# Kernel tuning notes

Measured on AMD Instinct MI355X. Metric: run time of the kernel, lower is better.

The kernel has to match this reference:

```python
import jax, jax.numpy as jnp
import numpy as np

N = 50000
E_RAND = 800000
E = E_RAND + N  # random edges + self loops
IN_DIM = 128
H = 4
D = 32  # num_hidden
HD = H * D  # 128
N_CLS = 2
NEG_SLOPE = 0.2
BN_EPS = 1e-5


def setup_inputs() -> dict:
    key = jax.random.key(0)
    ks = jax.random.split(key, 32)
    x = jax.random.randint(ks[0], (N,), 0, 200)
    src_r = jax.random.randint(ks[1], (E_RAND,), 0, N)
    dst_r = jax.random.randint(ks[2], (E_RAND,), 0, N)
    loops = jnp.arange(N)
    src = jnp.concatenate([src_r, loops])
    dst = jnp.concatenate([dst_r, loops])
    snorm_n = jax.random.uniform(ks[3], (N, 1), jnp.float32, 0.1, 1.0)
    snorm_e = jax.random.uniform(ks[4], (E, 1), jnp.float32, 0.1, 1.0)

    def nrm(k, shape, fan_in):
        return jax.random.normal(k, shape, jnp.float32) * (1.0 / np.sqrt(fan_in))

    inp = {
        'x': x, 'src': src, 'dst': dst, 'snorm_n': snorm_n, 'snorm_e': snorm_e,
        'embed': nrm(ks[5], (200, IN_DIM), 1.0),
        'W0': nrm(ks[6], (IN_DIM, HD), IN_DIM),
        'al0': nrm(ks[7], (H, D), D), 'ar0': nrm(ks[8], (H, D), D),
        'gamma0': jnp.ones((HD,), jnp.float32), 'beta0': jnp.zeros((HD,), jnp.float32),
        'W1': nrm(ks[9], (HD, HD), HD),
        'al1': nrm(ks[10], (H, D), D), 'ar1': nrm(ks[11], (H, D), D),
        'gamma1': jnp.ones((HD,), jnp.float32), 'beta1': jnp.zeros((HD,), jnp.float32),
        'W2': nrm(ks[12], (HD, HD), HD),
        'al2': nrm(ks[13], (H, D), D), 'ar2': nrm(ks[14], (H, D), D),
        'gamma2': jnp.ones((HD,), jnp.float32), 'beta2': jnp.zeros((HD,), jnp.float32),
        'cls1_w': nrm(ks[15], (HD, HD // 2), HD), 'cls1_b': jnp.zeros((HD // 2,), jnp.float32),
        'cls2_w': nrm(ks[16], (HD // 2, N_CLS), HD // 2), 'cls2_b': jnp.zeros((N_CLS,), jnp.float32),
    }
    return inp


def _gat_conv(h, W, al, ar, src, dst, residual, apply_act):
    # h: [N, F_in]; DGL-style GATConv with edge softmax over destination.
    feat = (h @ W).reshape(N, H, D)                         # [N,H,D]
    el = jnp.sum(feat * al, axis=-1)                        # [N,H]
    er = jnp.sum(feat * ar, axis=-1)                        # [N,H]
    e = jax.nn.leaky_relu(el[src] + er[dst], NEG_SLOPE)     # [E,H]
    m = jax.ops.segment_max(e, dst, num_segments=N)         # per-dst max
    ee = jnp.exp(e - m[dst])
    s = jax.ops.segment_sum(ee, dst, num_segments=N)
    a = ee / s[dst]                                         # edge softmax [E,H]
    msg = feat[src] * a[:, :, None]                         # [E,H,D]
    rst = jax.ops.segment_sum(msg, dst, num_segments=N)     # [N,H,D]
    if residual:
        rst = rst + h.reshape(N, H, D)  # identity residual (dims match)
    if apply_act:
        rst = jax.nn.elu(rst)           # activation inside GATConv (layers > 0)
    return rst.reshape(N, HD)


def _bn(h, gamma, beta):
    mu = jnp.mean(h, axis=0)
    var = jnp.mean((h - mu) ** 2, axis=0)  # biased var, matches torch BN training
    return gamma * (h - mu) * jax.lax.rsqrt(var + BN_EPS) + beta


def reference(x, src, dst, snorm_n, snorm_e, embed,
              W0, al0, ar0, gamma0, beta0,
              W1, al1, ar1, gamma1, beta1,
              W2, al2, ar2, gamma2, beta2,
              cls1_w, cls1_b, cls2_w, cls2_b):
    h = embed[x]  # [N, IN_DIM]
    layers = [
        (W0, al0, ar0, gamma0, beta0, False, False),
        (W1, al1, ar1, gamma1, beta1, True, True),
        (W2, al2, ar2, gamma2, beta2, True, True),
    ]
    for W, al, ar, g, b, res, act in layers:
        h = _gat_conv(h, W, al, ar, src, dst, res, act)
        h = h * snorm_n
        h = _bn(h, g, b)
        h = jax.nn.elu(h)
    h = jax.nn.relu(h @ cls1_w + cls1_b)
    logits = h @ cls2_w + cls2_b  # [N, N_CLS]
    return logits
```

## Files before the change

### kernel.cpp

```cpp
#include <hip/hip_runtime.h>
#include <hip/hip_bf16.h>
#include <hip/hip_fp16.h>
#include <math.h>

constexpr int N_NODES = 50000;
constexpr int N_EDGES = 850000;
constexpr int HDIM = 128;
constexpr int AGG_BLOCKS = N_NODES / 8;
constexpr int BN_BUCKETS = 16;

typedef _Float16 f16x8 __attribute__((ext_vector_type(8)));
typedef float f32x4 __attribute__((ext_vector_type(4)));

#define FMAMIX_LO(acc, pk, w) \
    asm("v_fma_mix_f32 %0, %1, %2, %0 op_sel:[0,0,0] op_sel_hi:[1,0,0]" \
        : "+v"(acc) : "v"(pk), "v"(w))
#define FMAMIX_HI(acc, pk, w) \
    asm("v_fma_mix_f32 %0, %1, %2, %0 op_sel:[1,0,0] op_sel_hi:[1,0,0]" \
        : "+v"(acc) : "v"(pk), "v"(w))

__device__ __forceinline__ float elu1(float t) {
    return (t > 0.f) ? t : (__expf(t) - 1.f);
}

constexpr int NB2 = 128;
constexpr int RANGE2 = (N_NODES + NB2 - 1) / NB2;
constexpr int CAP = 8192;
constexpr int CHUNK = 8192;
constexpr int GA = (N_EDGES + CHUNK - 1) / CHUNK;

__global__ void k_partA(const int* __restrict__ src, const int* __restrict__ dst,
                        int* __restrict__ g_cursor, unsigned* __restrict__ bucket) {
    __shared__ int hist[NB2];
    int tid = threadIdx.x;
    int e0 = blockIdx.x * CHUNK;
    int e1 = min(e0 + CHUNK, N_EDGES);
    if (tid < NB2) hist[tid] = 0;
    __syncthreads();
    for (int i = e0 + tid; i < e1; i += 1024) {
        int d = dst[i];
        atomicAdd(&hist[d / RANGE2], 1);
    }
    __syncthreads();
    int base = 0;
    if (tid < NB2) base = atomicAdd(&g_cursor[tid], hist[tid]);
    __syncthreads();
    if (tid < NB2) hist[tid] = base;
    __syncthreads();
    for (int i = e0 + tid; i < e1; i += 1024) {
        int d = dst[i];
        int s = src[i];
        int b = d / RANGE2;
        int p = atomicAdd(&hist[b], 1);
        bucket[b * CAP + p] = (unsigned)s | ((unsigned)(d - b * RANGE2) << 16);
    }
}

__global__ void k_partB(const unsigned* __restrict__ bucket, const int* __restrict__ cnts,
                        int* __restrict__ rowstart, int* __restrict__ esrc) {
    __shared__ int cnt_s[NB2];
    __shared__ int hist[RANGE2];
    __shared__ int lcur[RANGE2];
    __shared__ int wsum[7];
    int b = blockIdx.x, tid = threadIdx.x;
    int lo = b * RANGE2;
    int myCount = cnts[b];
    if (tid < NB2) cnt_s[tid] = cnts[tid];
    __syncthreads();
    for (int off = 1; off < NB2; off <<= 1) {
        int t = (tid < NB2 && tid >= off) ? cnt_s[tid - off] : 0;
        __syncthreads();
        if (tid < NB2) cnt_s[tid] += t;
        __syncthreads();
    }
    int base = cnt_s[b] - myCount;
    for (int j = tid; j < RANGE2; j += 1024) hist[j] = 0;
    __syncthreads();
    const unsigned* my = bucket + (size_t)b * CAP;
    for (int i = tid; i < myCount; i += 1024) atomicAdd(&hist[my[i] >> 16], 1);
    __syncthreads();
    int v = 0;
    if (tid < 448) v = (tid < RANGE2) ? hist[tid] : 0;
    int inc = v;
    int lane = tid & 63;
#pragma unroll
    for (int off = 1; off < 64; off <<= 1) {
        int t = __shfl_up(inc, off, 64);
        if (lane >= off) inc += t;
    }
    if (tid < 448 && lane == 63) wsum[tid >> 6] = inc;
    __syncthreads();
    if (tid < RANGE2) {
        int woff = 0;
        for (int w = 0; w < (tid >> 6); w++) woff += wsum[w];
        int excl = woff + inc - v;
        lcur[tid] = excl;
        int node = lo + tid;
        if (node < N_NODES) rowstart[node] = base + excl;
    }
    if (b == 0 && tid == 0) rowstart[N_NODES] = N_EDGES;
    __syncthreads();
    for (int i = tid; i < myCount; i += 1024) {
        unsigned p = my[i];
        int pos = atomicAdd(&lcur[p >> 16], 1);
        esrc[base + pos] = (int)(p & 0xFFFFu);
    }
}

__global__ void k_wpack(const float* __restrict__ W0, const float* __restrict__ W1,
                        const float* __restrict__ W2, __half* __restrict__ wpk,
                        float* __restrict__ bn_part, int* __restrict__ g_cursor) {
    int gid = blockIdx.x * 256 + threadIdx.x;
    {
        int z0 = gid * 8;
        if (z0 < 3 * BN_BUCKETS * 256) {
            float4 z = make_float4(0.f, 0.f, 0.f, 0.f);
            *reinterpret_cast<float4*>(&bn_part[z0]) = z;
            *reinterpret_cast<float4*>(&bn_part[z0 + 4]) = z;
        }
        if (gid < NB2) g_cursor[gid] = 0;
    }
    if (gid >= 3 * 2048) return;
    int L = gid >> 11;
    int rem = gid & 2047;
    int ct = rem >> 8;
    int kc = (rem >> 6) & 3;
    int l = rem & 63;
    const float* W = (L == 0) ? W0 : ((L == 1) ? W1 : W2);
    int c = ct * 16 + (l & 15);
    int k0 = kc * 32 + (l >> 4) * 8;
    __half tmp[8];
#pragma unroll
    for (int j = 0; j < 8; j++) tmp[j] = __float2half(W[(k0 + j) * HDIM + c]);
    *reinterpret_cast<float4*>(&wpk[((size_t)L << 14) + ((size_t)(ct * 4 + kc) * 64 + l) * 8]) =
        *reinterpret_cast<float4*>(tmp);
}

__global__ void k_gemm6(const __half* __restrict__ h, const int* __restrict__ xidx,
                        const float* __restrict__ embed, const f16x8* __restrict__ wB,
                        __half* __restrict__ feat_h, const float* __restrict__ bn_prev,
                        const float* __restrict__ gamma, const float* __restrict__ beta,
                        const float* __restrict__ al, const float* __restrict__ ar,
                        float* __restrict__ el, float* __restrict__ er, int mode) {
    __shared__ __half sf[4][16][136];
    __shared__ __align__(16) float s_sc[128];
    __shared__ __align__(16) float s_sh[128];
    int tid = threadIdx.x;
    if (mode != 0) {
        float* red = reinterpret_cast<float*>(sf);
        int c = tid & 127, which = tid >> 7;
        float t = 0.f;
#pragma unroll
        for (int b = 0; b < BN_BUCKETS; b++) t += bn_prev[b * 256 + which * 128 + c];
        red[tid] = t;
        __syncthreads();
        if (tid < 128) {
            float mu = red[tid] * (1.f / N_NODES);
            float var = red[128 + tid] * (1.f / N_NODES) - mu * mu;
            float sc = gamma[tid] * rsqrtf(var + 1e-5f);
            s_sc[tid] = sc;
            s_sh[tid] = beta[tid] - mu * sc;
        }
        __syncthreads();
    }
    int w = tid >> 6, lane = tid & 63;
    int r = lane & 15, kg = lane >> 4;
    int wbase = blockIdx.x * 64 + w * 16;
    int n = wbase + r;
    bool ok = n < N_NODES;

    f16x8 aF[4];
#pragma unroll
    for (int kc = 0; kc < 4; kc++)
#pragma unroll
        for (int j = 0; j < 8; j++) aF[kc][j] = (_Float16)0.f;
    if (ok) {
        if (mode == 0) {
            int xi = xidx[n];
            const float* ep = embed + (size_t)xi * HDIM;
#pragma unroll
            for (int kc = 0; kc < 4; kc++) {
                int c0 = kc * 32 + kg * 8;
                float4 e0 = *reinterpret_cast<const float4*>(ep + c0);
                float4 e1 = *reinterpret_cast<const float4*>(ep + c0 + 4);
                aF[kc][0] = (_Float16)e0.x; aF[kc][1] = (_Float16)e0.y;
                aF[kc][2] = (_Float16)e0.z; aF[kc][3] = (_Float16)e0.w;
                aF[kc][4] = (_Float16)e1.x; aF[kc][5] = (_Float16)e1.y;
                aF[kc][6] = (_Float16)e1.z; aF[kc][7] = (_Float16)e1.w;
            }
        } else {
            const __half* hp = h + (size_t)n * HDIM;
#pragma unroll
            for (int kc = 0; kc < 4; kc++) {
                int c0 = kc * 32 + kg * 8;
                float4 raw = *reinterpret_cast<const float4*>(hp + c0);
                const __half2* u = reinterpret_cast<const __half2*>(&raw);
                float4 sc0 = *reinterpret_cast<const float4*>(&s_sc[c0]);
                float4 sc1 = *reinterpret_cast<const float4*>(&s_sc[c0 + 4]);
                float4 sh0 = *reinterpret_cast<const float4*>(&s_sh[c0]);
                float4 sh1 = *reinterpret_cast<const float4*>(&s_sh[c0 + 4]);
                float scv[8] = {sc0.x, sc0.y, sc0.z, sc0.w, sc1.x, sc1.y, sc1.z, sc1.w};
                float shv[8] = {sh0.x, sh0.y, sh0.z, sh0.w, sh1.x, sh1.y, sh1.z, sh1.w};
                float vv[8];
#pragma unroll
                for (int t = 0; t < 4; t++) {
                    vv[2 * t] = __half2float(__low2half(u[t]));
                    vv[2 * t + 1] = __half2float(__high2half(u[t]));
                }
#pragma unroll
                for (int j = 0; j < 8; j++) {
                    float t = vv[j] * scv[j] + shv[j];
                    aF[kc][j] = (_Float16)elu1(t);
                }
            }
        }
    }
    if (mode != 0) __syncthreads();

    f32x4 acc[8] = {};
#pragma unroll
    for (int kc = 0; kc < 4; kc++) {
#pragma unroll
        for (int ct = 0; ct < 8; ct++) {
            f16x8 bF = wB[(ct * 4 + kc) * 64 + lane];
            acc[ct] = __builtin_amdgcn_mfma_f32_16x16x32_f16(aF[kc], bF, acc[ct], 0, 0, 0);
        }
    }

#pragma unroll
    for (int ct = 0; ct < 8; ct++)
#pragma unroll
        for (int reg = 0; reg < 4; reg++)
            sf[w][kg * 4 + reg][ct * 16 + r] = __float2half(acc[ct][reg]);
    __syncthreads();
#pragma unroll
    for (int q = 0; q < 4; q++) {
        int row = q * 4 + kg;
        int n2 = wbase + row;
        if (n2 < N_NODES) {
            float4 v = *reinterpret_cast<const float4*>(&sf[w][row][r * 8]);
            *reinterpret_cast<float4*>(&feat_h[(size_t)n2 * HDIM + r * 8]) = v;
        }
    }

    float alq[8], arq[8];
#pragma unroll
    for (int ct = 0; ct < 8; ct++) {
        alq[ct] = al[ct * 16 + r];
        arq[ct] = ar[ct * 16 + r];
    }
#pragma unroll
    for (int hd = 0; hd < 4; hd++) {
        float pl[4], pr[4];
#pragma unroll
        for (int reg = 0; reg < 4; reg++) {
            pl[reg] = acc[2 * hd][reg] * alq[2 * hd] + acc[2 * hd + 1][reg] * alq[2 * hd + 1];
            pr[reg] = acc[2 * hd][reg] * arq[2 * hd] + acc[2 * hd + 1][reg] * arq[2 * hd + 1];
        }
#pragma unroll
        for (int off = 1; off < 16; off <<= 1)
#pragma unroll
            for (int reg = 0; reg < 4; reg++) {
                pl[reg] += __shfl_xor(pl[reg], off, 64);
                pr[reg] += __shfl_xor(pr[reg], off, 64);
            }
        if (r == 0) {
#pragma unroll
            for (int reg = 0; reg < 4; reg++) {
                int n2 = wbase + kg * 4 + reg;
                if (n2 < N_NODES) {
                    el[n2 * 4 + hd] = pl[reg];
                    er[n2 * 4 + hd] = pr[reg];
                }
            }
        }
    }
}

__global__ void k_agg12(const __half* __restrict__ feat_h, const float* __restrict__ el,
                        const float* __restrict__ er, const int* __restrict__ rowstart,
                        const int* __restrict__ esrc, const float* __restrict__ snorm_n,
                        __half* __restrict__ h, const float* __restrict__ bn_prev,
                        const float* __restrict__ gamma, const float* __restrict__ beta,
                        float* __restrict__ bn_cur, int layer) {
    __shared__ __align__(16) int2 lds[4][2][2][32][4];
    __shared__ __align__(16) float s_sc[128];
    __shared__ __align__(16) float s_sh[128];
    int tid = threadIdx.x;
    if (layer > 0) {
        float* red = reinterpret_cast<float*>(lds);
        int c = tid & 127, which = tid >> 7;
        float t = 0.f;
#pragma unroll
        for (int b = 0; b < BN_BUCKETS; b++) t += bn_prev[b * 256 + which * 128 + c];
        red[tid] = t;
        __syncthreads();
        if (tid < 128) {
            float mu = red[tid] * (1.f / N_NODES);
            float var = red[128 + tid] * (1.f / N_NODES) - mu * mu;
            float sc = gamma[tid] * rsqrtf(var + 1e-5f);
            s_sc[tid] = sc;
            s_sh[tid] = beta[tid] - mu * sc;
        }
        __syncthreads();
    }
    int wave = tid >> 6, lane = tid & 63;
    int h2 = lane >> 5, hl = lane & 31;
    int dp = hl & 15, epair = hl >> 4, head = dp >> 2;
    unsigned dpo = (unsigned)dp << 4;
    const char* fb = reinterpret_cast<const char*>(feat_h);
    const char* eb = reinterpret_cast<const char*>(el);
    int n = blockIdx.x * 8 + wave * 2 + h2;
    int e0 = rowstart[n];
    int deg = rowstart[n + 1] - e0;
    int dmax = max(deg, __shfl_xor(deg, 32, 64));
    float4 er4 = *(const float4*)&er[n * 4];
    float s = 0.f;
    float a[8] = {};
    int nch = (dmax + 31) >> 5;

    int idx0 = e0 + min(hl, deg - 1);
    int sidx_p = esrc[idx0];
    float4 el_p = *reinterpret_cast<const float4*>(eb + ((unsigned)sidx_p << 4));
    bool val_p = hl < deg;

    for (int c = 0; c < nch; c++) {
        float w0 = 0.f, w1 = 0.f, w2 = 0.f, w3 = 0.f;
        int sv = sidx_p;
        if (val_p) {
            float ex = el_p.x + er4.x, ey = el_p.y + er4.y;
            float ez = el_p.z + er4.z, ew = el_p.w + er4.w;
            ex = fmaxf(ex, 0.f) + 0.2f * fminf(ex, 0.f);
            ey = fmaxf(ey, 0.f) + 0.2f * fminf(ey, 0.f);
            ez = fmaxf(ez, 0.f) + 0.2f * fminf(ez, 0.f);
            ew = fmaxf(ew, 0.f) + 0.2f * fminf(ew, 0.f);
            w0 = __expf(ex); w1 = __expf(ey); w2 = __expf(ez); w3 = __expf(ew);
        }
        int4* wp = reinterpret_cast<int4*>(&lds[wave][h2][c & 1][hl][0]);
        wp[0] = make_int4(sv, __float_as_int(w0), sv, __float_as_int(w1));
        wp[1] = make_int4(sv, __float_as_int(w2), sv, __float_as_int(w3));
        if (c + 1 < nch) {
            int slot = (c + 1) * 32 + hl;
            int idx = e0 + min(slot, deg - 1);
            sidx_p = esrc[idx];
            el_p = *reinterpret_cast<const float4*>(eb + ((unsigned)sidx_p << 4));
            val_p = slot < deg;
        }
        int cnt = min(32, dmax - c * 32);
        int iters = (cnt + 1) >> 1;
        const int2 (*slot_p)[4] = lds[wave][h2][c & 1];
        int j = 0;
#pragma unroll 1
        for (; j + 4 <= iters; j += 4) {
            int2 r0 = slot_p[(j + 0) * 2 + epair][head];
            int2 r1 = slot_p[(j + 1) * 2 + epair][head];
            int2 r2 = slot_p[(j + 2) * 2 + epair][head];
            int2 r3 = slot_p[(j + 3) * 2 + epair][head];
            uint4 u0 = *reinterpret_cast<const uint4*>(fb + (((unsigned)r0.x << 8) + dpo));
            uint4 u1 = *reinterpret_cast<const uint4*>(fb + (((unsigned)r1.x << 8) + dpo));
            uint4 u2 = *reinterpret_cast<const uint4*>(fb + (((unsigned)r2.x << 8) + dpo));
            uint4 u3 = *reinterpret_cast<const uint4*>(fb + (((unsigned)r3.x << 8) + dpo));
            float wa = __int_as_float(r0.y), wb = __int_as_float(r1.y);
            float wc = __int_as_float(r2.y), wd = __int_as_float(r3.y);
            FMAMIX_LO(a[0], u0.x, wa); FMAMIX_HI(a[1], u0.x, wa);
            FMAMIX_LO(a[2], u0.y, wa); FMAMIX_HI(a[3], u0.y, wa);
            FMAMIX_LO(a[4], u0.z, wa); FMAMIX_HI(a[5], u0.z, wa);
            FMAMIX_LO(a[6], u0.w, wa); FMAMIX_HI(a[7], u0.w, wa);
            FMAMIX_LO(a[0], u1.x, wb); FMAMIX_HI(a[1], u1.x, wb);
            FMAMIX_LO(a[2], u1.y, wb); FMAMIX_HI(a[3], u1.y, wb);
            FMAMIX_LO(a[4], u1.z, wb); FMAMIX_HI(a[5], u1.z, wb);
            FMAMIX_LO(a[6], u1.w, wb); FMAMIX_HI(a[7], u1.w, wb);
            FMAMIX_LO(a[0], u2.x, wc); FMAMIX_HI(a[1], u2.x, wc);
            FMAMIX_LO(a[2], u2.y, wc); FMAMIX_HI(a[3], u2.y, wc);
            FMAMIX_LO(a[4], u2.z, wc); FMAMIX_HI(a[5], u2.z, wc);
            FMAMIX_LO(a[6], u2.w, wc); FMAMIX_HI(a[7], u2.w, wc);
            FMAMIX_LO(a[0], u3.x, wd); FMAMIX_HI(a[1], u3.x, wd);
            FMAMIX_LO(a[2], u3.y, wd); FMAMIX_HI(a[3], u3.y, wd);
            FMAMIX_LO(a[4], u3.z, wd); FMAMIX_HI(a[5], u3.z, wd);
            FMAMIX_LO(a[6], u3.w, wd); FMAMIX_HI(a[7], u3.w, wd);
            s += (wa + wb) + (wc + wd);
        }
#pragma unroll 1
        for (; j < iters; j++) {
            int2 rec = slot_p[j * 2 + epair][head];
            float w = __int_as_float(rec.y);
            uint4 u = *reinterpret_cast<const uint4*>(fb + (((unsigned)rec.x << 8) + dpo));
            FMAMIX_LO(a[0], u.x, w); FMAMIX_HI(a[1], u.x, w);
            FMAMIX_LO(a[2], u.y, w); FMAMIX_HI(a[3], u.y, w);
            FMAMIX_LO(a[4], u.z, w); FMAMIX_HI(a[5], u.z, w);
            FMAMIX_LO(a[6], u.w, w); FMAMIX_HI(a[7], u.w, w);
            s += w;
        }
    }
#pragma unroll
    for (int k = 0; k < 8; k++) a[k] += __shfl_xor(a[k], 16, 64);
    s += __shfl_xor(s, 16, 64);
    float r[8] = {};
    if (epair == 0) {
        float inv = 1.f / s;
        int d0 = dp * 8;
#pragma unroll
        for (int k = 0; k < 8; k++) r[k] = a[k] * inv;
        if (layer > 0) {
            float4 hraw = *reinterpret_cast<const float4*>(&h[(size_t)n * HDIM + d0]);
            __half2 q0 = *(__half2*)&hraw.x, q1 = *(__half2*)&hraw.y;
            __half2 q2 = *(__half2*)&hraw.z, q3 = *(__half2*)&hraw.w;
            float hv[8] = {__half2float(__low2half(q0)), __half2float(__high2half(q0)),
                           __half2float(__low2half(q1)), __half2float(__high2half(q1)),
                           __half2float(__low2half(q2)), __half2float(__high2half(q2)),
                           __half2float(__low2half(q3)), __half2float(__high2half(q3))};
            float4 sc0 = *reinterpret_cast<const float4*>(&s_sc[d0]);
            float4 sc1 = *reinterpret_cast<const float4*>(&s_sc[d0 + 4]);
            float4 sh0 = *reinterpret_cast<const float4*>(&s_sh[d0]);
            float4 sh1 = *reinterpret_cast<const float4*>(&s_sh[d0 + 4]);
            float scv[8] = {sc0.x, sc0.y, sc0.z, sc0.w, sc1.x, sc1.y, sc1.z, sc1.w};
            float shv[8] = {sh0.x, sh0.y, sh0.z, sh0.w, sh1.x, sh1.y, sh1.z, sh1.w};
#pragma unroll
            for (int k = 0; k < 8; k++) {
                float t = hv[k] * scv[k] + shv[k];
                r[k] += elu1(t);
                r[k] = elu1(r[k]);
            }
        }
        float sn = snorm_n[n];
#pragma unroll
        for (int k = 0; k < 8; k++) r[k] *= sn;
        float4 outv;
        *(__half2*)&outv.x = __floats2half2_rn(r[0], r[1]);
        *(__half2*)&outv.y = __floats2half2_rn(r[2], r[3]);
        *(__half2*)&outv.z = __floats2half2_rn(r[4], r[5]);
        *(__half2*)&outv.w = __floats2half2_rn(r[6], r[7]);
        *reinterpret_cast<float4*>(&h[(size_t)n * HDIM + d0]) = outv;
    }

    float* bsum = reinterpret_cast<float*>(lds);
    __syncthreads();
    if (epair == 0) {
        int n8 = wave * 2 + h2;
        int cbase = n8 * 128 + dp * 8;
#pragma unroll
        for (int k = 0; k < 8; k++) {
            bsum[cbase + k] = r[k];
            bsum[1024 + cbase + k] = r[k] * r[k];
        }
    }
    __syncthreads();
    {
        int c = tid & 127, which = tid >> 7;
        float v = 0.f;
#pragma unroll
        for (int n8 = 0; n8 < 8; n8++) v += bsum[which * 1024 + n8 * 128 + c];
        atomicAdd(&bn_cur[(blockIdx.x & (BN_BUCKETS - 1)) * 256 + which * 128 + c], v);
    }
}

__global__ void k_classifier(const __half* __restrict__ h, const float* __restrict__ W1,
                             const float* __restrict__ b1, const float* __restrict__ W2,
                             const float* __restrict__ b2, const float* __restrict__ bn_prev,
                             const float* __restrict__ gamma, const float* __restrict__ beta,
                             float* __restrict__ out) {
    __shared__ float hs[16][128];
    __shared__ __align__(16) float s_sc[128];
    __shared__ __align__(16) float s_sh[128];
    int tid = threadIdx.x;
    {
        float* red = &hs[0][0];
        int c = tid & 127, which = tid >> 7;
        float t = 0.f;
#pragma unroll
        for (int b = 0; b < BN_BUCKETS; b++) t += bn_prev[b * 256 + which * 128 + c];
        red[tid] = t;
        __syncthreads();
        if (tid < 128) {
            float mu = red[tid] * (1.f / N_NODES);
            float var = red[128 + tid] * (1.f / N_NODES) - mu * mu;
            float sc = gamma[tid] * rsqrtf(var + 1e-5f);
            s_sc[tid] = sc;
            s_sh[tid] = beta[tid] - mu * sc;
        }
        __syncthreads();
    }
    int nbase = blockIdx.x * 16;
    for (int i = tid; i < 16 * 128; i += 256) {
        int r = i >> 7, c = i & 127;
        int n = nbase + r;
        float v = 0.f;
        if (n < N_NODES) {
            v = __half2float(h[(size_t)n * HDIM + c]) * s_sc[c] + s_sh[c];
            v = elu1(v);
        }
        hs[r][c] = v;
    }
    __syncthreads();
    int j = tid & 63;
    int g = tid >> 6;
    float bj = b1[j];
    float acc[4] = {bj, bj, bj, bj};
    for (int k = 0; k < 128; k++) {
        float w = W1[k * 64 + j];
#pragma unroll
        for (int i = 0; i < 4; i++) acc[i] += hs[g * 4 + i][k] * w;
    }
    float w20 = W2[j * 2], w21 = W2[j * 2 + 1];
    float res[8];
#pragma unroll
    for (int i = 0; i < 4; i++) {
        float hid = fmaxf(acc[i], 0.f);
        res[2 * i] = hid * w20;
        res[2 * i + 1] = hid * w21;
    }
#pragma unroll
    for (int off = 1; off < 64; off <<= 1)
#pragma unroll
        for (int i = 0; i < 8; i++) res[i] += __shfl_xor(res[i], off, 64);
    if (j < 8) {
        int n = nbase + g * 4 + (j >> 1);
        if (n < N_NODES) out[n * 2 + (j & 1)] = res[j] + b2[j & 1];
    }
}

extern "C" void kernel_launch(void* const* d_in, const int* in_sizes, int n_in,
                              void* d_out, int out_size, void* d_ws, size_t ws_size,
                              hipStream_t stream) {
    const int* x = (const int*)d_in[0];
    const int* src = (const int*)d_in[1];
    const int* dst = (const int*)d_in[2];
    const float* snorm_n = (const float*)d_in[3];
    const float* embed = (const float*)d_in[5];
    const float* Ws[3] = {(const float*)d_in[6], (const float*)d_in[11], (const float*)d_in[16]};
    const float* als[3] = {(const float*)d_in[7], (const float*)d_in[12], (const float*)d_in[17]};
    const float* ars[3] = {(const float*)d_in[8], (const float*)d_in[13], (const float*)d_in[18]};
    const float* gms[3] = {(const float*)d_in[9], (const float*)d_in[14], (const float*)d_in[19]};
    const float* bts[3] = {(const float*)d_in[10], (const float*)d_in[15], (const float*)d_in[20]};
    const float* cls1_w = (const float*)d_in[21];
    const float* cls1_b = (const float*)d_in[22];
    const float* cls2_w = (const float*)d_in[23];
    const float* cls2_b = (const float*)d_in[24];
    float* out = (float*)d_out;

    char* ws = (char*)d_ws;
    size_t off = 0;
    auto alloc = [&](size_t bytes) {
        void* p = ws + off;
        off = (off + bytes + 255) & ~(size_t)255;
        return p;
    };
    __half* h = (__half*)alloc((size_t)N_NODES * HDIM * 2);
    __half* feat_h = (__half*)alloc((size_t)N_NODES * HDIM * 2);
    float* el = (float*)alloc((size_t)N_NODES * 4 * 4);
    float* er = (float*)alloc((size_t)N_NODES * 4 * 4);
    int* rowstart = (int*)alloc((size_t)(N_NODES + 1) * 4);
    int* esrc = (int*)alloc((size_t)N_EDGES * 4);
    int* g_cursor = (int*)alloc((size_t)NB2 * 4);
    float* bn_part = (float*)alloc((size_t)3 * BN_BUCKETS * 256 * 4);
    __half* wpkh = (__half*)alloc((size_t)3 * 16384 * 2);
    unsigned* g_bucket = (unsigned*)feat_h;
    (void)ws_size; (void)in_sizes; (void)n_in; (void)out_size;

    k_wpack<<<(3 * 2048 + 255) / 256, 256, 0, stream>>>(Ws[0], Ws[1], Ws[2], wpkh,
                                                        bn_part, g_cursor);
    k_partA<<<GA, 1024, 0, stream>>>(src, dst, g_cursor, g_bucket);
    k_partB<<<NB2, 1024, 0, stream>>>(g_bucket, g_cursor, rowstart, esrc);

    for (int L = 0; L < 3; L++) {
        const f16x8* wB = reinterpret_cast<const f16x8*>(wpkh + ((size_t)L << 14));
        const float* bn_prev = bn_part + (size_t)(L == 0 ? 0 : L - 1) * BN_BUCKETS * 256;
        float* bn_cur = bn_part + (size_t)L * BN_BUCKETS * 256;
        int gprev = (L == 0) ? 0 : L - 1;
        k_gemm6<<<(N_NODES + 63) / 64, 256, 0, stream>>>(h, x, embed, wB, feat_h,
                                                         bn_prev, gms[gprev], bts[gprev],
                                                         als[L], ars[L], el, er, L == 0 ? 0 : 1);
        k_agg12<<<AGG_BLOCKS, 256, 0, stream>>>(feat_h, el, er, rowstart, esrc,
                                                snorm_n, h, bn_prev, gms[gprev], bts[gprev],
                                                bn_cur, L);
    }

    k_classifier<<<(N_NODES + 15) / 16, 256, 0, stream>>>(h, cls1_w, cls1_b, cls2_w, cls2_b,
                                                          bn_part + (size_t)2 * BN_BUCKETS * 256,
                                                          gms[2], bts[2], out);
}
```

Before: 330.9 us.

## Fuse CSR build with weight packing and layer-0 GEMM to cut launches

Merges edge bucketing with weight packing and BN-partial zeroing into one kernel. It also merges the CSR second pass with the layer-0 embedding GEMM into a single launch whose blocks pick a role by block index, so independent work runs concurrently. Because of this the bucket buffer now gets its own workspace allocation instead of aliasing feat_h. The el/er projection now comes from the fp16 values staged in LDS, using a shorter 4-lane shuffle reduction, and the cursor is cleared with a memset. The trade-offs are heterogeneous blocks in one launch, 1024-thread GEMM blocks, and slightly different rounding in el/er.

New measurement: 310.6 us. 1.07x faster.

```diff
diff --git a/kernel.cpp b/kernel.cpp
--- a/kernel.cpp
+++ b/kernel.cpp
@@ -28,154 +28,86 @@
 constexpr int CAP = 8192;
 constexpr int CHUNK = 8192;
 constexpr int GA = (N_EDGES + CHUNK - 1) / CHUNK;
-
-__global__ void k_partA(const int* __restrict__ src, const int* __restrict__ dst,
-                        int* __restrict__ g_cursor, unsigned* __restrict__ bucket) {
+constexpr int WPACK_BLOCKS = 6;
+constexpr int GEMM0_BLOCKS = (N_NODES + 255) / 256;
+constexpr int FUSEB_BLOCKS = GEMM0_BLOCKS + NB2;
+
+__global__ void k_fuseA(const int* __restrict__ src, const int* __restrict__ dst,
+                        int* __restrict__ g_cursor, unsigned* __restrict__ bucket,
+                        const float* __restrict__ W0, const float* __restrict__ W1,
+                        const float* __restrict__ W2, __half* __restrict__ wpk,
+                        float* __restrict__ bn_part) {
     __shared__ int hist[NB2];
     int tid = threadIdx.x;
-    int e0 = blockIdx.x * CHUNK;
-    int e1 = min(e0 + CHUNK, N_EDGES);
-    if (tid < NB2) hist[tid] = 0;
-    __syncthreads();
-    for (int i = e0 + tid; i < e1; i += 1024) {
-        int d = dst[i];
-        atomicAdd(&hist[d / RANGE2], 1);
-    }
-    __syncthreads();
-    int base = 0;
-    if (tid < NB2) base = atomicAdd(&g_cursor[tid], hist[tid]);
-    __syncthreads();
-    if (tid < NB2) hist[tid] = base;
-    __syncthreads();
-    for (int i = e0 + tid; i < e1; i += 1024) {
-        int d = dst[i];
-        int s = src[i];
-        int b = d / RANGE2;
-        int p = atomicAdd(&hist[b], 1);
-        bucket[b * CAP + p] = (unsigned)s | ((unsigned)(d - b * RANGE2) << 16);
-    }
-}
-
-__global__ void k_partB(const unsigned* __restrict__ bucket, const int* __restrict__ cnts,
-                        int* __restrict__ rowstart, int* __restrict__ esrc) {
-    __shared__ int cnt_s[NB2];
-    __shared__ int hist[RANGE2];
-    __shared__ int lcur[RANGE2];
-    __shared__ int wsum[7];
-    int b = blockIdx.x, tid = threadIdx.x;
-    int lo = b * RANGE2;
-    int myCount = cnts[b];
-    if (tid < NB2) cnt_s[tid] = cnts[tid];
-    __syncthreads();
-    for (int off = 1; off < NB2; off <<= 1) {
-        int t = (tid < NB2 && tid >= off) ? cnt_s[tid - off] : 0;
-        __syncthreads();
-        if (tid < NB2) cnt_s[tid] += t;
-        __syncthreads();
-    }
-    int base = cnt_s[b] - myCount;
-    for (int j = tid; j < RANGE2; j += 1024) hist[j] = 0;
-    __syncthreads();
-    const unsigned* my = bucket + (size_t)b * CAP;
-    for (int i = tid; i < myCount; i += 1024) atomicAdd(&hist[my[i] >> 16], 1);
-    __syncthreads();
-    int v = 0;
-    if (tid < 448) v = (tid < RANGE2) ? hist[tid] : 0;
-    int inc = v;
-    int lane = tid & 63;
-#pragma unroll
-    for (int off = 1; off < 64; off <<= 1) {
-        int t = __shfl_up(inc, off, 64);
-        if (lane >= off) inc += t;
-    }
-    if (tid < 448 && lane == 63) wsum[tid >> 6] = inc;
-    __syncthreads();
-    if (tid < RANGE2) {
-        int woff = 0;
-        for (int w = 0; w < (tid >> 6); w++) woff += wsum[w];
-        int excl = woff + inc - v;
-        lcur[tid] = excl;
-        int node = lo + tid;
-        if (node < N_NODES) rowstart[node] = base + excl;
-    }
-    if (b == 0 && tid == 0) rowstart[N_NODES] = N_EDGES;
-    __syncthreads();
-    for (int i = tid; i < myCount; i += 1024) {
-        unsigned p = my[i];
-        int pos = atomicAdd(&lcur[p >> 16], 1);
-        esrc[base + pos] = (int)(p & 0xFFFFu);
-    }
-}
-
-__global__ void k_wpack(const float* __restrict__ W0, const float* __restrict__ W1,
-                        const float* __restrict__ W2, __half* __restrict__ wpk,
-                        float* __restrict__ bn_part, int* __restrict__ g_cursor) {
-    int gid = blockIdx.x * 256 + threadIdx.x;
-    {
+    if (blockIdx.x < GA) {
+        int e0 = blockIdx.x * CHUNK;
+        int e1 = min(e0 + CHUNK, N_EDGES);
+        if (tid < NB2) hist[tid] = 0;
+        __syncthreads();
+        for (int i = e0 + tid; i < e1; i += 1024) {
+            int d = dst[i];
+            atomicAdd(&hist[d / RANGE2], 1);
+        }
+        __syncthreads();
+        int base = 0;
+        if (tid < NB2) base = atomicAdd(&g_cursor[tid], hist[tid]);
+        __syncthreads();
+        if (tid < NB2) hist[tid] = base;
+        __syncthreads();
+        for (int i = e0 + tid; i < e1; i += 1024) {
+            int d = dst[i];
+            int s = src[i];
+            int b = d / RANGE2;
+            int p = atomicAdd(&hist[b], 1);
+            bucket[b * CAP + p] = (unsigned)s | ((unsigned)(d - b * RANGE2) << 16);
+        }
+    } else {
+        int gid = (blockIdx.x - GA) * 1024 + tid;
         int z0 = gid * 8;
         if (z0 < 3 * BN_BUCKETS * 256) {
             float4 z = make_float4(0.f, 0.f, 0.f, 0.f);
             *reinterpret_cast<float4*>(&bn_part[z0]) = z;
             *reinterpret_cast<float4*>(&bn_part[z0 + 4]) = z;
         }
-        if (gid < NB2) g_cursor[gid] = 0;
-    }
-    if (gid >= 3 * 2048) return;
-    int L = gid >> 11;
-    int rem = gid & 2047;
-    int ct = rem >> 8;
-    int kc = (rem >> 6) & 3;
-    int l = rem & 63;
-    const float* W = (L == 0) ? W0 : ((L == 1) ? W1 : W2);
-    int c = ct * 16 + (l & 15);
-    int k0 = kc * 32 + (l >> 4) * 8;
-    __half tmp[8];
-#pragma unroll
-    for (int j = 0; j < 8; j++) tmp[j] = __float2half(W[(k0 + j) * HDIM + c]);
-    *reinterpret_cast<float4*>(&wpk[((size_t)L << 14) + ((size_t)(ct * 4 + kc) * 64 + l) * 8]) =
-        *reinterpret_cast<float4*>(tmp);
+        if (gid >= 3 * 2048) return;
+        int L = gid >> 11;
+        int rem = gid & 2047;
+        int ct = rem >> 8;
+        int kc = (rem >> 6) & 3;
+        int l = rem & 63;
+        const float* W = (L == 0) ? W0 : ((L == 1) ? W1 : W2);
+        int c = ct * 16 + (l & 15);
+        int k0 = kc * 32 + (l >> 4) * 8;
+        __half tmp[8];
+#pragma unroll
+        for (int j = 0; j < 8; j++) tmp[j] = __float2half(W[(k0 + j) * HDIM + c]);
+        *reinterpret_cast<float4*>(&wpk[((size_t)L << 14) +
+                                        ((size_t)(ct * 4 + kc) * 64 + l) * 8]) =
+            *reinterpret_cast<float4*>(tmp);
+    }
 }
 
-__global__ void k_gemm6(const __half* __restrict__ h, const int* __restrict__ xidx,
-                        const float* __restrict__ embed, const f16x8* __restrict__ wB,
-                        __half* __restrict__ feat_h, const float* __restrict__ bn_prev,
-                        const float* __restrict__ gamma, const float* __restrict__ beta,
+__global__ void k_fuseB(const int* __restrict__ xidx, const float* __restrict__ embed,
+                        const f16x8* __restrict__ wB, __half* __restrict__ feat_h,
                         const float* __restrict__ al, const float* __restrict__ ar,
-                        float* __restrict__ el, float* __restrict__ er, int mode) {
-    __shared__ __half sf[4][16][136];
-    __shared__ __align__(16) float s_sc[128];
-    __shared__ __align__(16) float s_sh[128];
+                        float* __restrict__ el, float* __restrict__ er,
+                        const unsigned* __restrict__ bucket, const int* __restrict__ cnts,
+                        int* __restrict__ rowstart, int* __restrict__ esrc) {
+    __shared__ __align__(16) char smem[16 * 16 * 136 * 2];
     int tid = threadIdx.x;
-    if (mode != 0) {
-        float* red = reinterpret_cast<float*>(sf);
-        int c = tid & 127, which = tid >> 7;
-        float t = 0.f;
-#pragma unroll
-        for (int b = 0; b < BN_BUCKETS; b++) t += bn_prev[b * 256 + which * 128 + c];
-        red[tid] = t;
-        __syncthreads();
-        if (tid < 128) {
-            float mu = red[tid] * (1.f / N_NODES);
-            float var = red[128 + tid] * (1.f / N_NODES) - mu * mu;
-            float sc = gamma[tid] * rsqrtf(var + 1e-5f);
-            s_sc[tid] = sc;
-            s_sh[tid] = beta[tid] - mu * sc;
-        }
-        __syncthreads();
-    }
-    int w = tid >> 6, lane = tid & 63;
-    int r = lane & 15, kg = lane >> 4;
-    int wbase = blockIdx.x * 64 + w * 16;
-    int n = wbase + r;
-    bool ok = n < N_NODES;
-
-    f16x8 aF[4];
-#pragma unroll
-    for (int kc = 0; kc < 4; kc++)
-#pragma unroll
-        for (int j = 0; j < 8; j++) aF[kc][j] = (_Float16)0.f;
-    if (ok) {
-        if (mode == 0) {
+    if (blockIdx.x < GEMM0_BLOCKS) {
+        __half (*sf)[16][136] = reinterpret_cast<__half (*)[16][136]>(smem);
+        int w = tid >> 6, lane = tid & 63;
+        int r = lane & 15, kg = lane >> 4;
+        int wbase = blockIdx.x * 256 + w * 16;
+        int n = wbase + r;
+        bool ok = n < N_NODES;
+        f16x8 aF[4];
+#pragma unroll
+        for (int kc = 0; kc < 4; kc++)
+#pragma unroll
+            for (int j = 0; j < 8; j++) aF[kc][j] = (_Float16)0.f;
+        if (ok) {
             int xi = xidx[n];
             const float* ep = embed + (size_t)xi * HDIM;
 #pragma unroll
@@ -188,34 +120,172 @@
                 aF[kc][4] = (_Float16)e1.x; aF[kc][5] = (_Float16)e1.y;
                 aF[kc][6] = (_Float16)e1.z; aF[kc][7] = (_Float16)e1.w;
             }
-        } else {
-            const __half* hp = h + (size_t)n * HDIM;
-#pragma unroll
-            for (int kc = 0; kc < 4; kc++) {
-                int c0 = kc * 32 + kg * 8;
-                float4 raw = *reinterpret_cast<const float4*>(hp + c0);
-                const __half2* u = reinterpret_cast<const __half2*>(&raw);
-                float4 sc0 = *reinterpret_cast<const float4*>(&s_sc[c0]);
-                float4 sc1 = *reinterpret_cast<const float4*>(&s_sc[c0 + 4]);
-                float4 sh0 = *reinterpret_cast<const float4*>(&s_sh[c0]);
-                float4 sh1 = *reinterpret_cast<const float4*>(&s_sh[c0 + 4]);
-                float scv[8] = {sc0.x, sc0.y, sc0.z, sc0.w, sc1.x, sc1.y, sc1.z, sc1.w};
-                float shv[8] = {sh0.x, sh0.y, sh0.z, sh0.w, sh1.x, sh1.y, sh1.z, sh1.w};
-                float vv[8];
-#pragma unroll
-                for (int t = 0; t < 4; t++) {
-                    vv[2 * t] = __half2float(__low2half(u[t]));
-                    vv[2 * t + 1] = __half2float(__high2half(u[t]));
-                }
-#pragma unroll
-                for (int j = 0; j < 8; j++) {
-                    float t = vv[j] * scv[j] + shv[j];
-                    aF[kc][j] = (_Float16)elu1(t);
-                }
+        }
+        f32x4 acc[8] = {};
+#pragma unroll
+        for (int kc = 0; kc < 4; kc++) {
+#pragma unroll
+            for (int ct = 0; ct < 8; ct++) {
+                f16x8 bF = wB[(ct * 4 + kc) * 64 + lane];
+                acc[ct] = __builtin_amdgcn_mfma_f32_16x16x32_f16(aF[kc], bF, acc[ct], 0, 0, 0);
             }
         }
-    }
-    if (mode != 0) __syncthreads();
+#pragma unroll
+        for (int ct = 0; ct < 8; ct++)
+#pragma unroll
+            for (int reg = 0; reg < 4; reg++)
+                sf[w][kg * 4 + reg][ct * 16 + r] = __float2half(acc[ct][reg]);
+        __syncthreads();
+        float alq[8], arq[8];
+        {
+            float4 a0 = *reinterpret_cast<const float4*>(&al[r * 8]);
+            float4 a1 = *reinterpret_cast<const float4*>(&al[r * 8 + 4]);
+            float4 b0 = *reinterpret_cast<const float4*>(&ar[r * 8]);
+            float4 b1 = *reinterpret_cast<const float4*>(&ar[r * 8 + 4]);
+            alq[0] = a0.x; alq[1] = a0.y; alq[2] = a0.z; alq[3] = a0.w;
+            alq[4] = a1.x; alq[5] = a1.y; alq[6] = a1.z; alq[7] = a1.w;
+            arq[0] = b0.x; arq[1] = b0.y; arq[2] = b0.z; arq[3] = b0.w;
+            arq[4] = b1.x; arq[5] = b1.y; arq[6] = b1.z; arq[7] = b1.w;
+        }
+#pragma unroll
+        for (int q = 0; q < 4; q++) {
+            int row = q * 4 + kg;
+            int n2 = wbase + row;
+            float4 v = *reinterpret_cast<const float4*>(&sf[w][row][r * 8]);
+            if (n2 < N_NODES)
+                *reinterpret_cast<float4*>(&feat_h[(size_t)n2 * HDIM + r * 8]) = v;
+            const __half2* u = reinterpret_cast<const __half2*>(&v);
+            float pl = 0.f, pr = 0.f;
+#pragma unroll
+            for (int t = 0; t < 4; t++) {
+                float lo = __half2float(__low2half(u[t]));
+                float hi = __half2float(__high2half(u[t]));
+                pl += lo * alq[2 * t] + hi * alq[2 * t + 1];
+                pr += lo * arq[2 * t] + hi * arq[2 * t + 1];
+            }
+            pl += __shfl_xor(pl, 1, 64); pr += __shfl_xor(pr, 1, 64);
+            pl += __shfl_xor(pl, 2, 64); pr += __shfl_xor(pr, 2, 64);
+            if ((r & 3) == 0 && n2 < N_NODES) {
+                int head = r >> 2;
+                el[n2 * 4 + head] = pl;
+                er[n2 * 4 + head] = pr;
+            }
+        }
+    } else {
+        int* cnt_s = reinterpret_cast<int*>(smem);
+        int* hist = cnt_s + NB2;
+        int* lcur = hist + RANGE2;
+        int* wsum = lcur + RANGE2;
+        int b = blockIdx.x - GEMM0_BLOCKS;
+        int lo = b * RANGE2;
+        int myCount = cnts[b];
+        if (tid < NB2) cnt_s[tid] = cnts[tid];
+        __syncthreads();
+        for (int off = 1; off < NB2; off <<= 1) {
+            int t = (tid < NB2 && tid >= off) ? cnt_s[tid - off] : 0;
+            __syncthreads();
+            if (tid < NB2) cnt_s[tid] += t;
+            __syncthreads();
+        }
+        int base = cnt_s[b] - myCount;
+        for (int j = tid; j < RANGE2; j += 1024) hist[j] = 0;
+        __syncthreads();
+        const unsigned* my = bucket + (size_t)b * CAP;
+        for (int i = tid; i < myCount; i += 1024) atomicAdd(&hist[my[i] >> 16], 1);
+        __syncthreads();
+        int v = 0;
+        if (tid < 448) v = (tid < RANGE2) ? hist[tid] : 0;
+        int inc = v;
+        int lane = tid & 63;
+#pragma unroll
+        for (int off = 1; off < 64; off <<= 1) {
+            int t = __shfl_up(inc, off, 64);
+            if (lane >= off) inc += t;
+        }
+        if (tid < 448 && lane == 63) wsum[tid >> 6] = inc;
+        __syncthreads();
+        if (tid < RANGE2) {
+            int woff = 0;
+            for (int w = 0; w < (tid >> 6); w++) woff += wsum[w];
+            int excl = woff + inc - v;
+            lcur[tid] = excl;
+            int node = lo + tid;
+            if (node < N_NODES) rowstart[node] = base + excl;
+        }
+        if (b == 0 && tid == 0) rowstart[N_NODES] = N_EDGES;
+        __syncthreads();
+        for (int i = tid; i < myCount; i += 1024) {
+            unsigned p = my[i];
+            int pos = atomicAdd(&lcur[p >> 16], 1);
+            esrc[base + pos] = (int)(p & 0xFFFFu);
+        }
+    }
+}
+
+__global__ void k_gemm6(const __half* __restrict__ h, const f16x8* __restrict__ wB,
+                        __half* __restrict__ feat_h, const float* __restrict__ bn_prev,
+                        const float* __restrict__ gamma, const float* __restrict__ beta,
+                        const float* __restrict__ al, const float* __restrict__ ar,
+                        float* __restrict__ el, float* __restrict__ er) {
+    __shared__ __half sf[4][16][136];
+    __shared__ __align__(16) float s_sc[128];
+    __shared__ __align__(16) float s_sh[128];
+    int tid = threadIdx.x;
+    {
+        float* red = reinterpret_cast<float*>(sf);
+        int c = tid & 127, which = tid >> 7;
+        float t = 0.f;
+#pragma unroll
+        for (int b = 0; b < BN_BUCKETS; b++) t += bn_prev[b * 256 + which * 128 + c];
+        red[tid] = t;
+        __syncthreads();
+        if (tid < 128) {
+            float mu = red[tid] * (1.f / N_NODES);
+            float var = red[128 + tid] * (1.f / N_NODES) - mu * mu;
+            float sc = gamma[tid] * rsqrtf(var + 1e-5f);
+            s_sc[tid] = sc;
+            s_sh[tid] = beta[tid] - mu * sc;
+        }
+        __syncthreads();
+    }
+    int w = tid >> 6, lane = tid & 63;
+    int r = lane & 15, kg = lane >> 4;
+    int wbase = blockIdx.x * 64 + w * 16;
+    int n = wbase + r;
+    bool ok = n < N_NODES;
+
+    f16x8 aF[4];
+#pragma unroll
+    for (int kc = 0; kc < 4; kc++)
+#pragma unroll
+        for (int j = 0; j < 8; j++) aF[kc][j] = (_Float16)0.f;
+    if (ok) {
+        const __half* hp = h + (size_t)n * HDIM;
+#pragma unroll
+        for (int kc = 0; kc < 4; kc++) {
+            int c0 = kc * 32 + kg * 8;
+            float4 raw = *reinterpret_cast<const float4*>(hp + c0);
+            const __half2* u = reinterpret_cast<const __half2*>(&raw);
+            float4 sc0 = *reinterpret_cast<const float4*>(&s_sc[c0]);
+            float4 sc1 = *reinterpret_cast<const float4*>(&s_sc[c0 + 4]);
+            float4 sh0 = *reinterpret_cast<const float4*>(&s_sh[c0]);
+            float4 sh1 = *reinterpret_cast<const float4*>(&s_sh[c0 + 4]);
+            float scv[8] = {sc0.x, sc0.y, sc0.z, sc0.w, sc1.x, sc1.y, sc1.z, sc1.w};
+            float shv[8] = {sh0.x, sh0.y, sh0.z, sh0.w, sh1.x, sh1.y, sh1.z, sh1.w};
+            float vv[8];
+#pragma unroll
+            for (int t = 0; t < 4; t++) {
+                vv[2 * t] = __half2float(__low2half(u[t]));
+                vv[2 * t + 1] = __half2float(__high2half(u[t]));
+            }
+#pragma unroll
+            for (int j = 0; j < 8; j++) {
+                float t = vv[j] * scv[j] + shv[j];
+                aF[kc][j] = (_Float16)elu1(t);
+            }
+        }
+    }
+    __syncthreads();
 
     f32x4 acc[8] = {};
 #pragma unroll
@@ -233,46 +303,39 @@
         for (int reg = 0; reg < 4; reg++)
             sf[w][kg * 4 + reg][ct * 16 + r] = __float2half(acc[ct][reg]);
     __syncthreads();
+    float alq[8], arq[8];
+    {
+        float4 a0 = *reinterpret_cast<const float4*>(&al[r * 8]);
+        float4 a1 = *reinterpret_cast<const float4*>(&al[r * 8 + 4]);
+        float4 b0 = *reinterpret_cast<const float4*>(&ar[r * 8]);
+        float4 b1 = *reinterpret_cast<const float4*>(&ar[r * 8 + 4]);
+        alq[0] = a0.x; alq[1] = a0.y; alq[2] = a0.z; alq[3] = a0.w;
+        alq[4] = a1.x; alq[5] = a1.y; alq[6] = a1.z; alq[7] = a1.w;
+        arq[0] = b0.x; arq[1] = b0.y; arq[2] = b0.z; arq[3] = b0.w;
+        arq[4] = b1.x; arq[5] = b1.y; arq[6] = b1.z; arq[7] = b1.w;
+    }
 #pragma unroll
     for (int q = 0; q < 4; q++) {
         int row = q * 4 + kg;
         int n2 = wbase + row;
-        if (n2 < N_NODES) {
-            float4 v = *reinterpret_cast<const float4*>(&sf[w][row][r * 8]);
+        float4 v = *reinterpret_cast<const float4*>(&sf[w][row][r * 8]);
+        if (n2 < N_NODES)
             *reinterpret_cast<float4*>(&feat_h[(size_t)n2 * HDIM + r * 8]) = v;
-        }
-    }
-
-    float alq[8], arq[8];
-#pragma unroll
-    for (int ct = 0; ct < 8; ct++) {
-        alq[ct] = al[ct * 16 + r];
-        arq[ct] = ar[ct * 16 + r];
-    }
-#pragma unroll
-    for (int hd = 0; hd < 4; hd++) {
-        float pl[4], pr[4];
-#pragma unroll
-        for (int reg = 0; reg < 4; reg++) {
-            pl[reg] = acc[2 * hd][reg] * alq[2 * hd] + acc[2 * hd + 1][reg] * alq[2 * hd + 1];
-            pr[reg] = acc[2 * hd][reg] * arq[2 * hd] + acc[2 * hd + 1][reg] * arq[2 * hd + 1];
-        }
-#pragma unroll
-        for (int off = 1; off < 16; off <<= 1)
-#pragma unroll
-            for (int reg = 0; reg < 4; reg++) {
-                pl[reg] += __shfl_xor(pl[reg], off, 64);
-                pr[reg] += __shfl_xor(pr[reg], off, 64);
-            }
-        if (r == 0) {
-#pragma unroll
-            for (int reg = 0; reg < 4; reg++) {
-                int n2 = wbase + kg * 4 + reg;
-                if (n2 < N_NODES) {
-                    el[n2 * 4 + hd] = pl[reg];
-                    er[n2 * 4 + hd] = pr[reg];
-                }
-            }
+        const __half2* u = reinterpret_cast<const __half2*>(&v);
+        float pl = 0.f, pr = 0.f;
+#pragma unroll
+        for (int t = 0; t < 4; t++) {
+            float lo = __half2float(__low2half(u[t]));
+            float hi = __half2float(__high2half(u[t]));
+            pl += lo * alq[2 * t] + hi * alq[2 * t + 1];
+            pr += lo * arq[2 * t] + hi * arq[2 * t + 1];
+        }
+        pl += __shfl_xor(pl, 1, 64); pr += __shfl_xor(pr, 1, 64);
+        pl += __shfl_xor(pl, 2, 64); pr += __shfl_xor(pr, 2, 64);
+        if ((r & 3) == 0 && n2 < N_NODES) {
+            int head = r >> 2;
+            el[n2 * 4 + head] = pl;
+            er[n2 * 4 + head] = pr;
         }
     }
 }
@@ -554,24 +617,28 @@
     int* g_cursor = (int*)alloc((size_t)NB2 * 4);
     float* bn_part = (float*)alloc((size_t)3 * BN_BUCKETS * 256 * 4);
     __half* wpkh = (__half*)alloc((size_t)3 * 16384 * 2);
-    unsigned* g_bucket = (unsigned*)feat_h;
+    unsigned* g_bucket = (unsigned*)alloc((size_t)NB2 * CAP * 4);
     (void)ws_size; (void)in_sizes; (void)n_in; (void)out_size;
 
-    k_wpack<<<(3 * 2048 + 255) / 256, 256, 0, stream>>>(Ws[0], Ws[1], Ws[2], wpkh,
-                                                        bn_part, g_cursor);
-    k_partA<<<GA, 1024, 0, stream>>>(src, dst, g_cursor, g_bucket);
-    k_partB<<<NB2, 1024, 0, stream>>>(g_bucket, g_cursor, rowstart, esrc);
-
-    for (int L = 0; L < 3; L++) {
+    hipMemsetAsync(g_cursor, 0, NB2 * 4, stream);
+    k_fuseA<<<GA + WPACK_BLOCKS, 1024, 0, stream>>>(src, dst, g_cursor, g_bucket,
+                                                    Ws[0], Ws[1], Ws[2], wpkh, bn_part);
+    k_fuseB<<<FUSEB_BLOCKS, 1024, 0, stream>>>(x, embed,
+                                               reinterpret_cast<const f16x8*>(wpkh),
+                                               feat_h, als[0], ars[0], el, er,
+                                               g_bucket, g_cursor, rowstart, esrc);
+    k_agg12<<<AGG_BLOCKS, 256, 0, stream>>>(feat_h, el, er, rowstart, esrc,
+                                            snorm_n, h, bn_part, gms[0], bts[0],
+                                            bn_part, 0);
+    for (int L = 1; L < 3; L++) {
         const f16x8* wB = reinterpret_cast<const f16x8*>(wpkh + ((size_t)L << 14));
-        const float* bn_prev = bn_part + (size_t)(L == 0 ? 0 : L - 1) * BN_BUCKETS * 256;
+        const float* bn_prev = bn_part + (size_t)(L - 1) * BN_BUCKETS * 256;
         float* bn_cur = bn_part + (size_t)L * BN_BUCKETS * 256;
-        int gprev = (L == 0) ? 0 : L - 1;
-        k_gemm6<<<(N_NODES + 63) / 64, 256, 0, stream>>>(h, x, embed, wB, feat_h,
-                                                         bn_prev, gms[gprev], bts[gprev],
-                                                         als[L], ars[L], el, er, L == 0 ? 0 : 1);
+        k_gemm6<<<(N_NODES + 63) / 64, 256, 0, stream>>>(h, wB, feat_h,
+                                                         bn_prev, gms[L - 1], bts[L - 1],
+                                                         als[L], ars[L], el, er);
         k_agg12<<<AGG_BLOCKS, 256, 0, stream>>>(feat_h, el, er, rowstart, esrc,
-                                                snorm_n, h, bn_prev, gms[gprev], bts[gprev],
+                                                snorm_n, h, bn_prev, gms[L - 1], bts[L - 1],
                                                 bn_cur, L);
     }
 
```
